# Optimization experiments

Hardware: AMD Instinct MI355X
Metric: run time of the kernel (lower is better)

The kernel has to match this reference:

```python
import jax, jax.numpy as jnp
import numpy as np

NUM_HEADS = 12
HEAD_DIM = 128
HIDDEN = 1536
SCALE = HEAD_DIM ** -0.5


def apply_rope(x, rope):
    # x: [B,H,S,D], rope: [S,1,D] -> freqs [S,D]
    freqs = rope[:, 0, :]
    cos = jnp.repeat(freqs[:, 0::2], 2, axis=-1)[None, None]  # [1,1,S,D]
    sin = jnp.repeat(freqs[:, 1::2], 2, axis=-1)[None, None]
    xr = x.reshape(*x.shape[:-1], -1, 2)
    x_real, x_imag = xr[..., 0], xr[..., 1]
    x_rot = jnp.stack([-x_imag, x_real], axis=-1).reshape(x.shape)
    return x * cos + x_rot * sin


def qkv_split(x, W):
    # x: [B,S,hidden], W: [3*H*D, hidden] (torch Linear layout)
    B, S, _ = x.shape
    y = (x @ W.T).reshape(B, S, 3, NUM_HEADS, HEAD_DIM).transpose(2, 0, 3, 1, 4)
    return y[0], y[1], y[2]  # each [B,H,S,D]


def sdpa(q, k, v):
    s = jnp.einsum('bhqd,bhkd->bhqk', q, k) * SCALE
    p = jax.nn.softmax(s, axis=-1)
    return jnp.einsum('bhqk,bhkd->bhqd', p, v)


def setup_inputs() -> dict:
    key = jax.random.key(0)
    ks = jax.random.split(key, 7)
    B, L, N = 1, 512, 4096
    txt = jax.random.normal(ks[0], (B, L, HIDDEN), dtype=jnp.float32)
    img = jax.random.normal(ks[1], (B, N, HIDDEN), dtype=jnp.float32)
    rope = jax.random.uniform(ks[2], (N, 1, HEAD_DIM), dtype=jnp.float32)
    s = 0.02
    W_txt_qkv = jax.random.normal(ks[3], (3 * NUM_HEADS * HEAD_DIM, HIDDEN), dtype=jnp.float32) * s
    W_img_qkv = jax.random.normal(ks[4], (3 * NUM_HEADS * HEAD_DIM, HIDDEN), dtype=jnp.float32) * s
    W_txt_out = jax.random.normal(ks[5], (HIDDEN, NUM_HEADS * HEAD_DIM), dtype=jnp.float32) * s
    W_img_out = jax.random.normal(ks[6], (HIDDEN, NUM_HEADS * HEAD_DIM), dtype=jnp.float32) * s
    return {'txt': txt, 'img': img, 'rope': rope, 'W_txt_qkv': W_txt_qkv,
            'W_img_qkv': W_img_qkv, 'W_txt_out': W_txt_out, 'W_img_out': W_img_out}


def reference(txt, img, rope, W_txt_qkv, W_img_qkv, W_txt_out, W_img_out):
    B, L, _ = txt.shape
    _, N, _ = img.shape
    txt_q, txt_k, txt_v = qkv_split(txt, W_txt_qkv)
    img_q, img_k, img_v = qkv_split(img, W_img_qkv)
    img_q = apply_rope(img_q, rope)
    img_k = apply_rope(img_k, rope)
    k = jnp.concatenate([txt_k, img_k], axis=2)  # [B,H,L+N,D]
    v = jnp.concatenate([txt_v, img_v], axis=2)
    txt_o = sdpa(txt_q, k, v).transpose(0, 2, 1, 3).reshape(B, L, -1)
    img_o = sdpa(img_q, k, v).transpose(0, 2, 1, 3).reshape(B, N, -1)
    return txt_o @ W_txt_out.T, img_o @ W_img_out.T
```

## Files before the change

### kernel.cpp

```cpp
#include <hip/hip_runtime.h>
#include <hip/hip_bf16.h>
#include <stdint.h>


typedef __attribute__((ext_vector_type(8)))  short bf16x8;
typedef __attribute__((ext_vector_type(4)))  float f32x4;
typedef __attribute__((ext_vector_type(16))) float f32x16;
typedef __attribute__((ext_vector_type(4)))  short s16x4;

#define NUM_HEADS 12
#define HEAD_DIM  128
#define HIDDEN    1536
#define LTXT      512
#define NIMG      4096
#define STOT      4608
#define QKV3      4608
#define SCALE_Q2  (0.08838834764831845f * 1.44269504088896340f)
#define DEFER_THR 12.0f

__device__ __forceinline__ float b2f(short s) {
    union { uint32_t u; float f; } c; c.u = ((uint32_t)(uint16_t)s) << 16; return c.f;
}
__device__ __forceinline__ short f2b(float f) {
    union { float f; uint32_t u; } c; c.f = f;
    uint32_t u = c.u + 0x7FFFu + ((c.u >> 16) & 1u);
    return (short)(u >> 16);
}
__device__ __forceinline__ float fexp2(float x) {
#if __has_builtin(__builtin_amdgcn_exp2f)
    return __builtin_amdgcn_exp2f(x);
#else
    return exp2f(x);
#endif
}
__device__ __forceinline__ uint32_t cvt_pk_bf16(float lo, float hi) {
    uint32_t r;
    asm("v_cvt_pk_bf16_f32 %0, %1, %2" : "=v"(r) : "v"(lo), "v"(hi));
    return r;
}
__device__ __forceinline__ void permlane32_swap(uint32_t& a, uint32_t& b) {
    asm("v_permlane32_swap_b32 %0, %1" : "+v"(a), "+v"(b));
}

typedef const void __attribute__((address_space(1)))* gas_p;
typedef void __attribute__((address_space(3)))* las_p;
__device__ __forceinline__ void gload_lds16(const void* g, void* l) {
    __builtin_amdgcn_global_load_lds((gas_p)g, (las_p)l, 16, 0, 0);
}

__global__ __launch_bounds__(256) void cast6(
    const float* __restrict__ s0, const float* __restrict__ s1,
    const float* __restrict__ s2, const float* __restrict__ s3,
    const float* __restrict__ s4, const float* __restrict__ s5,
    short* __restrict__ dst)
{
    size_t i = (size_t)blockIdx.x * 256 + threadIdx.x;
    const size_t e0 = 98304, e1 = 884736, e2 = 1769472,
                 e3 = 2654208, e4 = 2949120;
    const float* src; size_t base;
    if (i < e2) {
        if (i < e0)      { src = s0; base = 0;  }
        else if (i < e1) { src = s1; base = e0; }
        else             { src = s2; base = e1; }
    } else {
        if (i < e3)      { src = s3; base = e2; }
        else if (i < e4) { src = s4; base = e3; }
        else             { src = s5; base = e4; }
    }
    const float4* p = (const float4*)src + (i - base) * 2;
    float4 a = p[0], b = p[1];
    bf16x8 o;
    o[0] = f2b(a.x); o[1] = f2b(a.y); o[2] = f2b(a.z); o[3] = f2b(a.w);
    o[4] = f2b(b.x); o[5] = f2b(b.y); o[6] = f2b(b.z); o[7] = f2b(b.w);
    *((bf16x8*)dst + i) = o;
}

template <typename OT>
__global__ __launch_bounds__(256) void gemm_bt2(
    const short* __restrict__ A, const short* __restrict__ B0,
    const short* __restrict__ B1, OT* __restrict__ C,
    int M, int N, int K, int rowsplit)
{
    __shared__ __align__(16) short As[2][128 * 32];
    __shared__ __align__(16) short Bs[2][128 * 32];
    const int t    = threadIdx.x;
    const int lane = t & 63, wid = t >> 6;
    const int wr = wid >> 1, wc = wid & 1;
    const int l15 = lane & 15, lk = lane >> 4;
    const int bm = blockIdx.y, bn = blockIdx.x;

    const short* B = (bm * 128 < rowsplit) ? B0 : B1;
    const int srow = t >> 2, skg = t & 3;
    const short* Ag = A + (size_t)(bm * 128 + srow) * K + skg * 8;
    const short* Bg = B + (size_t)(bn * 128 + srow) * K + skg * 8;
    const size_t rowblk = (size_t)64 * K;

    f32x4 acc[4][4];
    const f32x4 z = {0.f, 0.f, 0.f, 0.f};
#pragma unroll
    for (int i = 0; i < 4; ++i)
#pragma unroll
        for (int j = 0; j < 4; ++j) acc[i][j] = z;

    auto STAGE = [&](int b, int kt) {
        const int k0 = kt * 32;
        gload_lds16(Ag + k0,          &As[b][wid * 512]);
        gload_lds16(Ag + rowblk + k0, &As[b][2048 + wid * 512]);
        gload_lds16(Bg + k0,          &Bs[b][wid * 512]);
        gload_lds16(Bg + rowblk + k0, &Bs[b][2048 + wid * 512]);
    };

    const int NT = K / 32;
    STAGE(0, 0);
    for (int kt = 0; kt < NT; ++kt) {
        const int cur = kt & 1;
        if (kt + 1 < NT) {
            STAGE(cur ^ 1, kt + 1);
            asm volatile("s_waitcnt vmcnt(4)" ::: "memory");
        } else {
            asm volatile("s_waitcnt vmcnt(0)" ::: "memory");
        }
        __builtin_amdgcn_s_barrier();

        bf16x8 af[4], bfr[4];
#pragma unroll
        for (int i = 0; i < 4; ++i)
            af[i] = *(const bf16x8*)&As[cur][(wr * 64 + i * 16 + l15) * 32 + lk * 8];
#pragma unroll
        for (int j = 0; j < 4; ++j)
            bfr[j] = *(const bf16x8*)&Bs[cur][(wc * 64 + j * 16 + l15) * 32 + lk * 8];
        __builtin_amdgcn_s_setprio(1);
#pragma unroll
        for (int i = 0; i < 4; ++i)
#pragma unroll
            for (int j = 0; j < 4; ++j)
                acc[i][j] = __builtin_amdgcn_mfma_f32_16x16x32_bf16(
                    af[i], bfr[j], acc[i][j], 0, 0, 0);
        __builtin_amdgcn_s_setprio(0);

        asm volatile("s_waitcnt lgkmcnt(0)" ::: "memory");
        __builtin_amdgcn_sched_barrier(0);
        __builtin_amdgcn_s_barrier();
    }

#pragma unroll
    for (int i = 0; i < 4; ++i) {
#pragma unroll
        for (int j = 0; j < 4; ++j) {
            const int row0 = bm * 128 + wr * 64 + i * 16 + lk * 4;
            const int col  = bn * 128 + wc * 64 + j * 16 + l15;
#pragma unroll
            for (int r = 0; r < 4; ++r) {
                float v = acc[i][j][r];
                if constexpr (sizeof(OT) == 2)
                    C[(size_t)(row0 + r) * N + col] = (OT)f2b(v);
                else
                    C[(size_t)(row0 + r) * N + col] = v;
            }
        }
    }
}

__global__ __launch_bounds__(256) void pack_qkv(
    const short* __restrict__ Y, const float* __restrict__ rope,
    short* __restrict__ Qb, short* __restrict__ Kb, short* __restrict__ VTb)
{
    const int st = blockIdx.x, h = blockIdx.y, t = threadIdx.x;
    const int s0 = st * 64;
    __shared__ __align__(16) short Vt[128][72];

#pragma unroll
    for (int i = 0; i < 4; ++i) {
        int e  = t + i * 256;
        int sl = e >> 4, dg = e & 15;
        int s  = s0 + sl;
        const short* src = Y + (size_t)s * QKV3;
        bf16x8 q8 = *(const bf16x8*)(src + h * 128 + dg * 8);
        bf16x8 k8 = *(const bf16x8*)(src + (12 + h) * 128 + dg * 8);
        bf16x8 v8 = *(const bf16x8*)(src + (24 + h) * 128 + dg * 8);
        float qf[8], kf[8];
#pragma unroll
        for (int j = 0; j < 8; ++j) { qf[j] = b2f(q8[j]); kf[j] = b2f(k8[j]); }
        if (s >= LTXT) {
            const float* rp = rope + (size_t)(s - LTXT) * 128 + dg * 8;
            float4 r0 = *(const float4*)rp;
            float4 r1 = *(const float4*)(rp + 4);
            float rr[8] = {r0.x, r0.y, r0.z, r0.w, r1.x, r1.y, r1.z, r1.w};
#pragma unroll
            for (int j = 0; j < 4; ++j) {
                float c = rr[2 * j], sn = rr[2 * j + 1];
                float q0 = qf[2 * j], q1 = qf[2 * j + 1];
                qf[2 * j] = q0 * c - q1 * sn; qf[2 * j + 1] = q1 * c + q0 * sn;
                float k0 = kf[2 * j], k1 = kf[2 * j + 1];
                kf[2 * j] = k0 * c - k1 * sn; kf[2 * j + 1] = k1 * c + k0 * sn;
            }
        }
        bf16x8 qo, ko;
#pragma unroll
        for (int j = 0; j < 8; ++j) { qo[j] = f2b(qf[j] * SCALE_Q2); ko[j] = f2b(kf[j]); }
        *(bf16x8*)(Qb + ((size_t)h * STOT + s) * 128 + dg * 8) = qo;
        *(bf16x8*)(Kb + ((size_t)h * STOT + s) * 128 + dg * 8) = ko;
#pragma unroll
        for (int j = 0; j < 8; ++j) Vt[dg * 8 + j][sl] = v8[j];
    }
    __syncthreads();
#pragma unroll
    for (int i = 0; i < 4; ++i) {
        int c = t + i * 256;
        int d = c >> 3, sg = c & 7;
        bf16x8 val = *(const bf16x8*)&Vt[d][sg * 8];
        *(bf16x8*)(VTb + ((size_t)h * 128 + d) * STOT + s0 + sg * 8) = val;
    }
}

__global__ __launch_bounds__(512, 2) void attn_fwd(
    const short* __restrict__ Q, const short* __restrict__ Kb,
    const short* __restrict__ VT, short* __restrict__ O)
{
    const int id  = blockIdx.x;
    const int swz = (id & 7) * 27 + (id >> 3);
    const int qb  = swz % 18, h = swz / 18;

    const int t = threadIdx.x;
    const int lane = t & 63, wid = t >> 6;
    const int l31 = lane & 31, hi = lane >> 5;
    const int xorb = l31 & 7;

    __shared__ __align__(16) short KV[3][2][64 * 128];

    const short* Qrow = Q + ((size_t)h * STOT + qb * 256 + wid * 32 + l31) * 128;
    bf16x8 qf[8];
#pragma unroll
    for (int dk = 0; dk < 8; ++dk)
        qf[dk] = *(const bf16x8*)(Qrow + dk * 16 + hi * 8);

    f32x16 o[4];
#pragma unroll
    for (int nt = 0; nt < 4; ++nt)
#pragma unroll
        for (int r = 0; r < 16; ++r) o[nt][r] = 0.f;
    float m = -1e30f, den = 0.f;

    const short* Kh = Kb + (size_t)h * STOT * 128;
    const short* Vh = VT + (size_t)h * 128 * STOT;

    const short* Ksrc[2]; const short* Vsrc[2];
#pragma unroll
    for (int i = 0; i < 2; ++i) {
        int p = t + i * 512;
        int krow = p >> 4, kx = (p & 15) ^ (krow & 7);
        Ksrc[i] = Kh + (size_t)krow * 128 + kx * 8;
        int vrow = p >> 3, vx = (p & 7) ^ (vrow & 7);
        Vsrc[i] = Vh + (size_t)vrow * STOT + vx * 8;
    }

    auto STAGE = [&](int b, int kb) {
#pragma unroll
        for (int i = 0; i < 2; ++i) {
            gload_lds16(Ksrc[i] + (size_t)kb * 8192, &KV[b][0][i * 4096 + wid * 512]);
            gload_lds16(Vsrc[i] + (size_t)kb * 64,   &KV[b][1][i * 4096 + wid * 512]);
        }
    };

    int kaddr[8], vaddr[4];
#pragma unroll
    for (int dk = 0; dk < 8; ++dk)
        kaddr[dk] = l31 * 256 + (((dk * 2 + hi) ^ xorb) << 4);
#pragma unroll
    for (int s = 0; s < 4; ++s)
        vaddr[s] = l31 * 128 + (((s * 2 + hi) ^ xorb) << 4);

    const char* Kbase[3] = { (const char*)&KV[0][0][0], (const char*)&KV[1][0][0],
                             (const char*)&KV[2][0][0] };
    const char* Vbase[3] = { (const char*)&KV[0][1][0], (const char*)&KV[1][1][0],
                             (const char*)&KV[2][1][0] };

    auto TILE = [&](const char* Ksc, const char* Vsc) {
        f32x16 sc0, sc1;
#pragma unroll
        for (int r = 0; r < 16; ++r) { sc0[r] = 0.f; sc1[r] = 0.f; }
        __builtin_amdgcn_s_setprio(1);
#pragma unroll
        for (int dk = 0; dk < 8; ++dk) {
            bf16x8 kf0 = *(const bf16x8*)(Ksc + kaddr[dk]);
            bf16x8 kf1 = *(const bf16x8*)(Ksc + kaddr[dk] + 8192);
            sc0 = __builtin_amdgcn_mfma_f32_32x32x16_bf16(kf0, qf[dk], sc0, 0, 0, 0);
            sc1 = __builtin_amdgcn_mfma_f32_32x32x16_bf16(kf1, qf[dk], sc1, 0, 0, 0);
        }
        __builtin_amdgcn_s_setprio(0);

        float v = sc0[0];
#pragma unroll
        for (int r = 1; r < 16; ++r) v = fmaxf(v, sc0[r]);
#pragma unroll
        for (int r = 0; r < 16; ++r) v = fmaxf(v, sc1[r]);
        v = fmaxf(v, __shfl_xor(v, 32));
        if (__any(v > m + DEFER_THR)) {
            float mn = fmaxf(m, v);
            float al = fexp2(m - mn);
            m = mn;
            den *= al;
#pragma unroll
            for (int nt = 0; nt < 4; ++nt)
#pragma unroll
                for (int r = 0; r < 16; ++r) o[nt][r] *= al;
        }
        float rs = 0.f;
#pragma unroll
        for (int r = 0; r < 16; ++r) { sc0[r] = fexp2(sc0[r] - m); rs += sc0[r]; }
#pragma unroll
        for (int r = 0; r < 16; ++r) { sc1[r] = fexp2(sc1[r] - m); rs += sc1[r]; }
        rs += __shfl_xor(rs, 32);
        den += rs;

        __builtin_amdgcn_s_setprio(1);
#pragma unroll
        for (int s = 0; s < 4; ++s) {
            const f32x16& pe = (s < 2) ? sc0 : sc1;
            const int rb = (s & 1) * 8;
            uint32_t a0 = cvt_pk_bf16(pe[rb + 0], pe[rb + 1]);
            uint32_t a1 = cvt_pk_bf16(pe[rb + 2], pe[rb + 3]);
            uint32_t a2 = cvt_pk_bf16(pe[rb + 4], pe[rb + 5]);
            uint32_t a3 = cvt_pk_bf16(pe[rb + 6], pe[rb + 7]);
            permlane32_swap(a0, a2);
            permlane32_swap(a1, a3);
            union { uint32_t u[4]; bf16x8 v8; } pb;
            pb.u[0] = a0; pb.u[1] = a1; pb.u[2] = a2; pb.u[3] = a3;
#pragma unroll
            for (int nt = 0; nt < 4; ++nt) {
                bf16x8 vf = *(const bf16x8*)(Vsc + vaddr[s] + nt * 4096);
                o[nt] = __builtin_amdgcn_mfma_f32_32x32x16_bf16(vf, pb.v8, o[nt], 0, 0, 0);
            }
        }
        __builtin_amdgcn_s_setprio(0);
    };

    const int NT = STOT / 64;
    STAGE(0, 0);
    for (int kb3 = 0; kb3 < NT; kb3 += 3) {
        STAGE(1, kb3 + 1);
        asm volatile("s_waitcnt vmcnt(4)" ::: "memory");
        __builtin_amdgcn_s_barrier();
        TILE(Kbase[0], Vbase[0]);

        STAGE(2, kb3 + 2);
        asm volatile("s_waitcnt vmcnt(4)" ::: "memory");
        __builtin_amdgcn_s_barrier();
        TILE(Kbase[1], Vbase[1]);

        if (kb3 + 3 < NT) {
            STAGE(0, kb3 + 3);
            asm volatile("s_waitcnt vmcnt(4)" ::: "memory");
        } else {
            asm volatile("s_waitcnt vmcnt(0)" ::: "memory");
        }
        __builtin_amdgcn_s_barrier();
        TILE(Kbase[2], Vbase[2]);
    }

    const int qrow = qb * 256 + wid * 32 + l31;
    float inv = 1.0f / den;
    short* Orow = O + (size_t)qrow * HIDDEN + h * 128;
#pragma unroll
    for (int nt = 0; nt < 4; ++nt) {
#pragma unroll
        for (int g = 0; g < 4; ++g) {
            s16x4 w4;
#pragma unroll
            for (int j = 0; j < 4; ++j) w4[j] = f2b(o[nt][g * 4 + j] * inv);
            *(s16x4*)(Orow + nt * 32 + g * 8 + hi * 4) = w4;
        }
    }
}

extern "C" void kernel_launch(void* const* d_in, const int* in_sizes, int n_in,
                              void* d_out, int out_size, void* d_ws, size_t ws_size,
                              hipStream_t stream)
{
    (void)in_sizes; (void)n_in; (void)out_size; (void)ws_size;
    const float* txt  = (const float*)d_in[0];
    const float* img  = (const float*)d_in[1];
    const float* rope = (const float*)d_in[2];
    const float* Wtq  = (const float*)d_in[3];
    const float* Wiq  = (const float*)d_in[4];
    const float* Wto  = (const float*)d_in[5];
    const float* Wio  = (const float*)d_in[6];
    float* out = (float*)d_out;

    short* w = (short*)d_ws;
    size_t off = 0;
    auto alloc = [&](size_t elems) { short* p = w + off; off += elems; return p; };
    short* txtb = alloc((size_t)LTXT * HIDDEN);
    short* imgb = alloc((size_t)NIMG * HIDDEN);
    short* Wtqb = alloc((size_t)QKV3 * HIDDEN);
    short* Wiqb = alloc((size_t)QKV3 * HIDDEN);
    short* Wtob = alloc((size_t)HIDDEN * HIDDEN);
    short* Wiob = alloc((size_t)HIDDEN * HIDDEN);
    short* Yt   = alloc((size_t)LTXT * QKV3);
    short* Yi   = alloc((size_t)NIMG * QKV3);
    short* Qb   = alloc((size_t)NUM_HEADS * STOT * HEAD_DIM);
    short* Kb   = alloc((size_t)NUM_HEADS * STOT * HEAD_DIM);
    short* VTb  = alloc((size_t)NUM_HEADS * STOT * HEAD_DIM);
    (void)imgb; (void)Yi;
    short* Ob   = txtb;

    cast6<<<12672, 256, 0, stream>>>(txt, img, Wtq, Wiq, Wto, Wio, txtb);

    gemm_bt2<short><<<dim3(QKV3 / 128, STOT / 128), 256, 0, stream>>>(
        txtb, Wtqb, Wiqb, Yt, STOT, QKV3, HIDDEN, LTXT);

    pack_qkv<<<dim3(STOT / 64, NUM_HEADS), 256, 0, stream>>>(
        Yt, rope, Qb, Kb, VTb);

    attn_fwd<<<dim3(STOT / 256 * NUM_HEADS), 512, 0, stream>>>(Qb, Kb, VTb, Ob);

    gemm_bt2<float><<<dim3(HIDDEN / 128, STOT / 128), 256, 0, stream>>>(
        Ob, Wtob, Wiob, out, STOT, HIDDEN, HIDDEN, LTXT);
}
```

Before: 307.7 us.

## Software-pipeline attention: overlap next tile's QK^T with current softmax/PV

Splits the per-tile attention body into a QK^T stage and a softmax+PV stage and interleaves them, so the score MFMAs for tile j+1 are issued before the softmax and PV of tile j. The LDS ring grows from three to four K/V buffers so the extra tile in flight stays resident. This aims to hide exp/max latency behind matrix work, at the cost of a second set of score registers (pressure at 2 waves/SIMD launch bounds) and more LDS, which can lower occupancy.

```diff
diff --git a/kernel.cpp b/kernel.cpp
--- a/kernel.cpp
+++ b/kernel.cpp
@@ -226,7 +226,7 @@
     const int l31 = lane & 31, hi = lane >> 5;
     const int xorb = l31 & 7;
 
-    __shared__ __align__(16) short KV[3][2][64 * 128];
+    __shared__ __align__(16) short KV[4][2][64 * 128];
 
     const short* Qrow = Q + ((size_t)h * STOT + qb * 256 + wid * 32 + l31) * 128;
     bf16x8 qf[8];
@@ -270,30 +270,31 @@
     for (int s = 0; s < 4; ++s)
         vaddr[s] = l31 * 128 + (((s * 2 + hi) ^ xorb) << 4);
 
-    const char* Kbase[3] = { (const char*)&KV[0][0][0], (const char*)&KV[1][0][0],
-                             (const char*)&KV[2][0][0] };
-    const char* Vbase[3] = { (const char*)&KV[0][1][0], (const char*)&KV[1][1][0],
-                             (const char*)&KV[2][1][0] };
-
-    auto TILE = [&](const char* Ksc, const char* Vsc) {
-        f32x16 sc0, sc1;
-#pragma unroll
-        for (int r = 0; r < 16; ++r) { sc0[r] = 0.f; sc1[r] = 0.f; }
+    const char* Kb4[4] = { (const char*)&KV[0][0][0], (const char*)&KV[1][0][0],
+                           (const char*)&KV[2][0][0], (const char*)&KV[3][0][0] };
+    const char* Vb4[4] = { (const char*)&KV[0][1][0], (const char*)&KV[1][1][0],
+                           (const char*)&KV[2][1][0], (const char*)&KV[3][1][0] };
+
+    auto QK = [&](const char* Ksc, f32x16& s0, f32x16& s1) {
+#pragma unroll
+        for (int r = 0; r < 16; ++r) { s0[r] = 0.f; s1[r] = 0.f; }
         __builtin_amdgcn_s_setprio(1);
 #pragma unroll
         for (int dk = 0; dk < 8; ++dk) {
             bf16x8 kf0 = *(const bf16x8*)(Ksc + kaddr[dk]);
             bf16x8 kf1 = *(const bf16x8*)(Ksc + kaddr[dk] + 8192);
-            sc0 = __builtin_amdgcn_mfma_f32_32x32x16_bf16(kf0, qf[dk], sc0, 0, 0, 0);
-            sc1 = __builtin_amdgcn_mfma_f32_32x32x16_bf16(kf1, qf[dk], sc1, 0, 0, 0);
+            s0 = __builtin_amdgcn_mfma_f32_32x32x16_bf16(kf0, qf[dk], s0, 0, 0, 0);
+            s1 = __builtin_amdgcn_mfma_f32_32x32x16_bf16(kf1, qf[dk], s1, 0, 0, 0);
         }
         __builtin_amdgcn_s_setprio(0);
-
-        float v = sc0[0];
-#pragma unroll
-        for (int r = 1; r < 16; ++r) v = fmaxf(v, sc0[r]);
-#pragma unroll
-        for (int r = 0; r < 16; ++r) v = fmaxf(v, sc1[r]);
+    };
+
+    auto SMPV = [&](const char* Vsc, f32x16& s0, f32x16& s1) {
+        float v = s0[0];
+#pragma unroll
+        for (int r = 1; r < 16; ++r) v = fmaxf(v, s0[r]);
+#pragma unroll
+        for (int r = 0; r < 16; ++r) v = fmaxf(v, s1[r]);
         v = fmaxf(v, __shfl_xor(v, 32));
         if (__any(v > m + DEFER_THR)) {
             float mn = fmaxf(m, v);
@@ -307,16 +308,16 @@
         }
         float rs = 0.f;
 #pragma unroll
-        for (int r = 0; r < 16; ++r) { sc0[r] = fexp2(sc0[r] - m); rs += sc0[r]; }
-#pragma unroll
-        for (int r = 0; r < 16; ++r) { sc1[r] = fexp2(sc1[r] - m); rs += sc1[r]; }
+        for (int r = 0; r < 16; ++r) { s0[r] = fexp2(s0[r] - m); rs += s0[r]; }
+#pragma unroll
+        for (int r = 0; r < 16; ++r) { s1[r] = fexp2(s1[r] - m); rs += s1[r]; }
         rs += __shfl_xor(rs, 32);
         den += rs;
 
         __builtin_amdgcn_s_setprio(1);
 #pragma unroll
         for (int s = 0; s < 4; ++s) {
-            const f32x16& pe = (s < 2) ? sc0 : sc1;
+            const f32x16& pe = (s < 2) ? s0 : s1;
             const int rb = (s & 1) * 8;
             uint32_t a0 = cvt_pk_bf16(pe[rb + 0], pe[rb + 1]);
             uint32_t a1 = cvt_pk_bf16(pe[rb + 2], pe[rb + 3]);
@@ -335,28 +336,57 @@
         __builtin_amdgcn_s_setprio(0);
     };
 
-    const int NT = STOT / 64;
+    f32x16 scA0, scA1, scB0, scB1;
+
     STAGE(0, 0);
-    for (int kb3 = 0; kb3 < NT; kb3 += 3) {
-        STAGE(1, kb3 + 1);
+    STAGE(1, 1);
+    asm volatile("s_waitcnt vmcnt(4)" ::: "memory");
+    __builtin_amdgcn_s_barrier();
+    QK(Kb4[0], scA0, scA1);
+
+    for (int jb = 0; jb < 68; jb += 4) {
+        STAGE(2, jb + 2);
         asm volatile("s_waitcnt vmcnt(4)" ::: "memory");
         __builtin_amdgcn_s_barrier();
-        TILE(Kbase[0], Vbase[0]);
-
-        STAGE(2, kb3 + 2);
+        QK(Kb4[1], scB0, scB1);
+        SMPV(Vb4[0], scA0, scA1);
+
+        STAGE(3, jb + 3);
         asm volatile("s_waitcnt vmcnt(4)" ::: "memory");
         __builtin_amdgcn_s_barrier();
-        TILE(Kbase[1], Vbase[1]);
-
-        if (kb3 + 3 < NT) {
-            STAGE(0, kb3 + 3);
-            asm volatile("s_waitcnt vmcnt(4)" ::: "memory");
-        } else {
-            asm volatile("s_waitcnt vmcnt(0)" ::: "memory");
-        }
-        __builtin_amdgcn_s_barrier();
-        TILE(Kbase[2], Vbase[2]);
-    }
+        QK(Kb4[2], scA0, scA1);
+        SMPV(Vb4[1], scB0, scB1);
+
+        STAGE(0, jb + 4);
+        asm volatile("s_waitcnt vmcnt(4)" ::: "memory");
+        __builtin_amdgcn_s_barrier();
+        QK(Kb4[3], scB0, scB1);
+        SMPV(Vb4[2], scA0, scA1);
+
+        STAGE(1, jb + 5);
+        asm volatile("s_waitcnt vmcnt(4)" ::: "memory");
+        __builtin_amdgcn_s_barrier();
+        QK(Kb4[0], scA0, scA1);
+        SMPV(Vb4[3], scB0, scB1);
+    }
+    STAGE(2, 70);
+    asm volatile("s_waitcnt vmcnt(4)" ::: "memory");
+    __builtin_amdgcn_s_barrier();
+    QK(Kb4[1], scB0, scB1);
+    SMPV(Vb4[0], scA0, scA1);
+
+    STAGE(3, 71);
+    asm volatile("s_waitcnt vmcnt(4)" ::: "memory");
+    __builtin_amdgcn_s_barrier();
+    QK(Kb4[2], scA0, scA1);
+    SMPV(Vb4[1], scB0, scB1);
+
+    asm volatile("s_waitcnt vmcnt(0)" ::: "memory");
+    __builtin_amdgcn_s_barrier();
+    QK(Kb4[3], scB0, scB1);
+    SMPV(Vb4[2], scA0, scA1);
+
+    SMPV(Vb4[3], scB0, scB1);
 
     const int qrow = qb * 256 + wid * 32 + l31;
     float inv = 1.0f / den;
```

After: 301.5 us. -2.0%, faster.
